# Optimization experiments

Measured on AMD Instinct MI355X. Metric: run time of the kernel, lower is better.

The kernel has to match this reference:

```python
import jax, jax.numpy as jnp
import numpy as np
from jax import lax

B = 32  # CS block size


def _conv(x, w, stride=1, pad=0):
    return lax.conv_general_dilated(
        x, w, window_strides=(stride, stride),
        padding=[(pad, pad), (pad, pad)],
        dimension_numbers=("NCHW", "OIHW", "NCHW"))


def _prelu(x, a):
    return jnp.where(x >= 0, x, a * x)


def _reshape_concat(x):
    # x: [N, B*B, h, w]; channel c = j*B + i maps to block pixel (i, j)
    # (tmp.view(B,B).permute(1,0) in the torch code). Blocks tile rows by
    # dim2 (h) and cols by dim3 (w). Vectorized depth-to-space + transpose.
    N, C, h, w = x.shape
    x5 = x.reshape(N, B, B, h, w)            # dims: (N, j, i, h, w)
    x5 = jnp.transpose(x5, (0, 3, 2, 4, 1))  # (N, h, i, w, j)
    return x5.reshape(N, 1, h * B, w * B)


def setup_inputs() -> dict:
    key = jax.random.key(0)
    ks = jax.random.split(key, 6)
    N, H, W = 16, 256, 256
    csnb = int(0.25 * B * B)  # 256
    inp = {
        "x": jax.random.normal(ks[0], (N, 1, H, W), jnp.float32),
        "W_cs": jax.random.normal(ks[1], (csnb, 1, B, B), jnp.float32) * 0.03,
        "W_init": jax.random.normal(ks[2], (B * B, csnb, 1, 1), jnp.float32) * 0.06,
        "W_first": jax.random.normal(ks[3], (64, 1, 3, 3), jnp.float32) * 0.3,
        "W_blk": jax.random.normal(ks[4], (64, 64, 3, 3), jnp.float32) * 0.04,
        "W_last": jax.random.normal(ks[5], (1, 64, 3, 3), jnp.float32) * 0.04,
        "a_main": jnp.full((1,), 0.1, jnp.float32),
        "a_blk": jnp.full((1,), 0.1, jnp.float32),
    }
    return inp


def reference(x, W_cs, W_init, W_first, W_blk, W_last, a_main, a_blk):
    # CS sampling: [N,1,H,W] -> [N,csnb,H/B,W/B]
    outcsy = _conv(x, W_cs, stride=B, pad=0)
    # initial reconstruction: 1x1 conv to B*B channels
    out = _conv(outcsy, W_init, stride=1, pad=0)
    out_initrec = _reshape_concat(out)          # [N,1,H,W]
    out = _prelu(_conv(out_initrec, W_first, pad=1), a_main)
    # same SORTRes_block (shared weights) applied 4 times
    for _ in range(4):
        o1 = _conv(out, W_blk, pad=1)
        o2 = _prelu(o1, a_blk)
        o3 = _conv(o2, W_blk, pad=1)
        out = _prelu(out + o3, a_blk)
    out = _conv(out + out_initrec, W_last, pad=1)
    return (out, outcsy, out_initrec)
```

## Files before the change

### kernel.cpp

```cpp
#include <hip/hip_runtime.h>
#include <hip/hip_bf16.h>
#include <initializer_list>


#define HW 65536
#define IMG 4194304

typedef __attribute__((ext_vector_type(8))) short short8;
typedef __attribute__((ext_vector_type(4))) float f32x4;

__device__ __forceinline__ float bf2f(unsigned short u) {
    union { unsigned u; float f; } v; v.u = ((unsigned)u) << 16; return v.f;
}
__device__ __forceinline__ unsigned short f2bf(float f) {
    union { float f; unsigned u; } v; v.f = f;
    unsigned r = v.u + 0x7FFF + ((v.u >> 16) & 1);
    return (unsigned short)(r >> 16);
}

__global__ void k_wcsT(const float* __restrict__ Wcs, float* __restrict__ WT)
{
    int e = blockIdx.x * 256 + threadIdx.x;
    int k = e >> 8, c = e & 255;
    WT[(long)k * 256 + c] = Wcs[(long)c * 1024 + k];
}

__global__ void k_winitT(const float* __restrict__ Wi, float* __restrict__ WT)
{
    int e = blockIdx.x * 256 + threadIdx.x;
    int ci = e >> 10, cc = e & 1023;
    WT[e] = Wi[(long)cc * 256 + ci];
}

__global__ __launch_bounds__(256) void k_cs2(const float* __restrict__ x,
        const float* __restrict__ WT, float* __restrict__ outcsy)
{
    __shared__ float xs[2][1024];
    const int b = blockIdx.x;
    const int tid = threadIdx.x;
#pragma unroll
    for (int t = 0; t < 2; ++t) {
        int p = b * 2 + t;
        int wb = p & 7, hb = (p >> 3) & 7, n = p >> 6;
#pragma unroll
        for (int i = 0; i < 4; ++i) {
            int k = tid + 256 * i;
            int ii = k >> 5, jj = k & 31;
            xs[t][k] = x[(long)n * HW + (hb * 32 + ii) * 256 + wb * 32 + jj];
        }
    }
    __syncthreads();
    float a0 = 0.f, a1 = 0.f;
    for (int k = 0; k < 1024; k += 8) {
#pragma unroll
        for (int u = 0; u < 8; ++u) {
            float wv = WT[(long)(k + u) * 256 + tid];
            a0 += wv * xs[0][k + u];
            a1 += wv * xs[1][k + u];
        }
    }
#pragma unroll
    for (int t = 0; t < 2; ++t) {
        int p = b * 2 + t;
        int wb = p & 7, hb = (p >> 3) & 7, n = p >> 6;
        float a = t ? a1 : a0;
        outcsy[(long)n * 16384 + tid * 64 + hb * 8 + wb] = a;
    }
}

__global__ __launch_bounds__(256) void k_init2(const float* __restrict__ outcsy,
        const float* __restrict__ WT, float* __restrict__ initrec)
{
    __shared__ float ys[2][256];
    __shared__ float ov[2][1024];
    const int b = blockIdx.x;
    const int np = b & 7, s = b >> 3;
    const int wb = s & 7, hb = s >> 3;
    const int tid = threadIdx.x;
#pragma unroll
    for (int i = 0; i < 2; ++i) {
        int idx = tid + 256 * i;
        int t = idx >> 8, c = idx & 255;
        ys[t][c] = outcsy[(long)(np * 2 + t) * 16384 + c * 64 + s];
    }
    __syncthreads();
#pragma unroll
    for (int q4 = 0; q4 < 4; ++q4) {
        int cc = q4 * 256 + tid;
        float a0 = 0.f, a1 = 0.f;
        for (int ci = 0; ci < 256; ci += 8) {
#pragma unroll
            for (int u = 0; u < 8; ++u) {
                float wv = WT[(long)(ci + u) * 1024 + cc];
                a0 += wv * ys[0][ci + u];
                a1 += wv * ys[1][ci + u];
            }
        }
        int i = cc & 31, j = cc >> 5;
        ov[0][i * 32 + j] = a0;
        ov[1][i * 32 + j] = a1;
    }
    __syncthreads();
#pragma unroll
    for (int t = 0; t < 2; ++t) {
        int n = np * 2 + t;
#pragma unroll
        for (int i2 = 0; i2 < 4; ++i2) {
            int p = i2 * 256 + tid;
            int i = p >> 5, j = p & 31;
            initrec[(long)n * HW + (hb * 32 + i) * 256 + wb * 32 + j] = ov[t][p];
        }
    }
}

__global__ __launch_bounds__(256) void k_first(const float* __restrict__ initrec,
        const float* __restrict__ Wf, unsigned short* __restrict__ A,
        const float* __restrict__ alpha_p)
{
    const int tid = threadIdx.x;
    const int w = tid >> 6, lane = tid & 63;
    const long p0 = (long)blockIdx.x * 64 + w * 16;
    const int n = (int)(p0 >> 16);
    const int y = (int)((p0 >> 8) & 255);
    const int xb = (int)(p0 & 255);
    float wf[9];
#pragma unroll
    for (int k = 0; k < 9; ++k) wf[k] = Wf[lane * 9 + k];
    const float alpha = alpha_p[0];
    const float* ip = initrec + (long)n * HW;
    for (int i = 0; i < 16; ++i) {
        int x = xb + i;
        float acc = 0.f;
#pragma unroll
        for (int ky = 0; ky < 3; ++ky) {
            int yy = y + ky - 1;
            if ((unsigned)yy >= 256u) continue;
#pragma unroll
            for (int kx = 0; kx < 3; ++kx) {
                int xx = x + kx - 1;
                if ((unsigned)xx >= 256u) continue;
                acc += wf[ky * 3 + kx] * ip[yy * 256 + xx];
            }
        }
        acc = acc >= 0.f ? acc : alpha * acc;
        A[(p0 + i) * 64 + lane] = f2bf(acc);
    }
}

__global__ void k_wprep(const float* __restrict__ Wb, unsigned short* __restrict__ Wp)
{
    int e = blockIdx.x * 256 + threadIdx.x;
    int cc = e / 18432, r = e % 18432;
    int tap = r / 2048, r2 = r % 2048;
    int nt = (r2 >> 9) & 3, l = (r2 >> 3) & 63, j = r2 & 7;
    int co = nt * 16 + (l & 15);
    int ci = cc * 32 + (l >> 4) * 8 + j;
    Wp[e] = f2bf(Wb[co * 576 + ci * 9 + tap]);
}

template <int MODE>
__global__ __launch_bounds__(256, 3) void k_conv(const unsigned short* __restrict__ src,
        const unsigned short* __restrict__ res, unsigned short* __restrict__ dst,
        const unsigned short* __restrict__ Wp, const float* __restrict__ alpha_p)
{
    __shared__ short halo[23328];

    const int tid = threadIdx.x;
    const int bid = blockIdx.x;
    const int tx = bid & 15, ty = (bid >> 4) & 15, n = bid >> 8;
    const int x0 = tx * 16, y0 = ty * 16;
    const int w = tid >> 6, lane = tid & 63;
    const int q = lane >> 4, mm = lane & 15;

    const unsigned short* sb = src + (long)n * IMG;
#pragma unroll
    for (int i = 0; i < 11; ++i) {
        int idx = tid + 256 * i;
        if (idx < 2592) {
            int pix = idx >> 3, part = idx & 7;
            int row = pix / 18, col = pix - row * 18;
            int gy = y0 + row - 1, gx = x0 + col - 1;
            short8 v = {0, 0, 0, 0, 0, 0, 0, 0};
            if ((unsigned)gy < 256u && (unsigned)gx < 256u)
                v = *(const short8*)&sb[((long)gy * 256 + gx) * 64 + part * 8];
            *(short8*)&halo[pix * 72 + part * 8] = v;
        }
    }

    short8 bcur[4], bnxt[4];
#pragma unroll
    for (int nt = 0; nt < 4; ++nt)
        bcur[nt] = *(const short8*)&Wp[(size_t)(nt * 512 + lane * 8)];

    const f32x4 zz = {0.f, 0.f, 0.f, 0.f};
    f32x4 acc[4][4];
#pragma unroll
    for (int mt = 0; mt < 4; ++mt)
#pragma unroll
        for (int nt = 0; nt < 4; ++nt) acc[mt][nt] = zz;

    __syncthreads();

    const int mmt = mm * 72 + q * 8;
#pragma unroll
    for (int s = 0; s < 18; ++s) {
        const int cc = s / 9, tap = s % 9;
        const int ky = tap / 3, kx = tap % 3;
        const int sn = (s + 1 < 18) ? s + 1 : s;
        const int ccn = sn / 9, tapn = sn % 9;
#pragma unroll
        for (int nt = 0; nt < 4; ++nt)
            bnxt[nt] = *(const short8*)&Wp[(size_t)ccn * 18432 +
                                           (size_t)((tapn * 4 + nt) * 512 + lane * 8)];
        const int soff = ky * 1296 + kx * 72 + cc * 32 + mmt;
#pragma unroll
        for (int mt = 0; mt < 4; ++mt) {
            short8 af = *(const short8*)&halo[(4 * w + mt) * 1296 + soff];
#pragma unroll
            for (int nt = 0; nt < 4; ++nt)
                acc[mt][nt] = __builtin_amdgcn_mfma_f32_16x16x32_bf16(
                    af, bcur[nt], acc[mt][nt], 0, 0, 0);
        }
#pragma unroll
        for (int nt = 0; nt < 4; ++nt) bcur[nt] = bnxt[nt];
    }
    __syncthreads();

    unsigned short* ob = (unsigned short*)halo;
    const float alpha = alpha_p[0];
#pragma unroll
    for (int h = 0; h < 2; ++h) {
        if ((w >> 1) == h) {
#pragma unroll
            for (int mt = 0; mt < 4; ++mt) {
                int row = 4 * w + mt - 8 * h;
#pragma unroll
                for (int nt = 0; nt < 4; ++nt)
#pragma unroll
                    for (int r = 0; r < 4; ++r) {
                        int xx = q * 4 + r;
                        ob[(row * 16 + xx) * 64 + nt * 16 + mm] = f2bf(acc[mt][nt][r]);
                    }
            }
        }
        __syncthreads();
#pragma unroll
        for (int i = 0; i < 4; ++i) {
            int e = (tid + 256 * i) * 8;
            int co = e & 63, xx = (e >> 6) & 15, row = 8 * h + (e >> 10);
            long g = (((long)n * 256 + y0 + row) * 256 + (x0 + xx)) * 64 + co;
            short8 cv = *(short8*)&ob[e];
            short8 rv = {0, 0, 0, 0, 0, 0, 0, 0};
            if (MODE == 1) rv = *(const short8*)&res[g];
            short8 ov;
#pragma unroll
            for (int j = 0; j < 8; ++j) {
                float v = bf2f((unsigned short)cv[j]);
                if (MODE == 1) v += bf2f((unsigned short)rv[j]);
                v = (v >= 0.f) ? v : alpha * v;
                ov[j] = (short)f2bf(v);
            }
            *(short8*)&dst[g] = ov;
        }
        __syncthreads();
    }
}

__global__ __launch_bounds__(256) void k_last(const unsigned short* __restrict__ A,
        const float* __restrict__ initrec, const float* __restrict__ Wl,
        float* __restrict__ out0)
{
    __shared__ short ibuf[23328];
    const int bid = blockIdx.x;
    const int tx = bid & 15, ty = (bid >> 4) & 15, n = bid >> 8;
    const int x0 = tx * 16, y0 = ty * 16;
    const int tid = threadIdx.x;
    const unsigned short* Ab = A + (long)n * IMG;

#pragma unroll
    for (int i = 0; i < 11; ++i) {
        int idx = tid + 256 * i;
        if (idx < 2592) {
            int pix = idx >> 3, part = idx & 7;
            int row = pix / 18, col = pix - row * 18;
            int gy = y0 + row - 1, gx = x0 + col - 1;
            short8 v = {0, 0, 0, 0, 0, 0, 0, 0};
            if ((unsigned)gy < 256u && (unsigned)gx < 256u)
                v = *(const short8*)&Ab[((long)gy * 256 + gx) * 64 + part * 8];
            *(short8*)&ibuf[pix * 72 + part * 8] = v;
        }
    }
    __syncthreads();

    float wsum[9];
#pragma unroll
    for (int k = 0; k < 9; ++k) wsum[k] = 0.f;
    for (int ci = 0; ci < 64; ++ci)
#pragma unroll
        for (int k = 0; k < 9; ++k) wsum[k] += Wl[ci * 9 + k];

    const int x = tid & 15, y = tid >> 4;
    const float* ip = initrec + (long)n * HW;
    float acc = 0.f;
#pragma unroll
    for (int ky = 0; ky < 3; ++ky) {
#pragma unroll
        for (int kx = 0; kx < 3; ++kx) {
            const int tap = ky * 3 + kx;
            const short* p = &ibuf[((y + ky) * 18 + (x + kx)) * 72];
#pragma unroll
            for (int c8 = 0; c8 < 8; ++c8) {
                short8 av = *(const short8*)&p[c8 * 8];
#pragma unroll
                for (int j = 0; j < 8; ++j)
                    acc += Wl[(c8 * 8 + j) * 9 + tap] * bf2f((unsigned short)av[j]);
            }
            int gy = y0 + y + ky - 1, gx = x0 + x + kx - 1;
            if ((unsigned)gy < 256u && (unsigned)gx < 256u)
                acc += wsum[tap] * ip[gy * 256 + gx];
        }
    }
    out0[((long)n * 256 + y0 + y) * 256 + (x0 + x)] = acc;
}

extern "C" void kernel_launch(void* const* d_in, const int* in_sizes, int n_in,
                              void* d_out, int out_size, void* d_ws, size_t ws_size,
                              hipStream_t stream)
{
    const float* x     = (const float*)d_in[0];
    const float* Wcs   = (const float*)d_in[1];
    const float* Winit = (const float*)d_in[2];
    const float* Wf    = (const float*)d_in[3];
    const float* Wb    = (const float*)d_in[4];
    const float* Wl    = (const float*)d_in[5];
    const float* amain = (const float*)d_in[6];
    const float* ablk  = (const float*)d_in[7];

    float* out0    = (float*)d_out;
    float* outcsy  = out0 + 1048576;
    float* initrec = outcsy + 262144;

    const size_t EXTRA = 73728 + 2 * 1048576;
    unsigned short* A = (unsigned short*)d_ws;
    int nc = 1;
    for (int c : {16, 8, 4, 2, 1})
        if ((size_t)(16 + c) * IMG * 2 + EXTRA <= ws_size) { nc = c; break; }
    unsigned short* Bt   = A + (size_t)16 * IMG;
    unsigned short* Wp   = Bt + (size_t)nc * IMG;
    float*          WcsT = (float*)(Wp + 36864);
    float*          WinT = WcsT + 262144;

    k_wcsT<<<1024, 256, 0, stream>>>(Wcs, WcsT);
    k_winitT<<<1024, 256, 0, stream>>>(Winit, WinT);
    k_wprep<<<144, 256, 0, stream>>>(Wb, Wp);

    k_cs2<<<512, 256, 0, stream>>>(x, WcsT, outcsy);
    k_init2<<<512, 256, 0, stream>>>(outcsy, WinT, initrec);
    k_first<<<16384, 256, 0, stream>>>(initrec, Wf, A, amain);

    for (int i = 0; i < 4; ++i) {
        for (int n0 = 0; n0 < 16; n0 += nc) {
            unsigned short* Ac = A + (size_t)n0 * IMG;
            k_conv<0><<<nc * 256, 256, 0, stream>>>(Ac, (const unsigned short*)nullptr,
                                                    Bt, Wp, ablk);
            k_conv<1><<<nc * 256, 256, 0, stream>>>(Bt, Ac, Ac, Wp, ablk);
        }
    }
    k_last<<<4096, 256, 0, stream>>>(A, initrec, Wl, out0);
}
```

Before: 1.235 ms.

## Fuse both convolutions of each residual block into one kernel with recomputed halo

Replaces the two per-block conv launches with a single kernel that loads a 20x20 halo tile in two 32-channel halves. It computes the first conv plus PReLU over an 18x18 region into shared memory, then runs the second conv from that buffer and applies the residual add and PReLU. This drops the global write and reread of the intermediate activation, and the blocks now ping-pong between two buffers. The cost is recomputing the halo ring (about 27% extra MFMA work on the first conv), more shared memory and lower occupancy. k_first is also rewritten so each thread handles one pixel and all 64 channels, writing them with vectorized 16-byte stores.

Result: faster. 1.125 ms (-9.0%).

```diff
diff --git a/kernel.cpp b/kernel.cpp
--- a/kernel.cpp
+++ b/kernel.cpp
@@ -117,33 +117,37 @@
         const float* __restrict__ Wf, unsigned short* __restrict__ A,
         const float* __restrict__ alpha_p)
 {
+    const int bid = blockIdx.x;
+    const int tx = bid & 15, ty = (bid >> 4) & 15, n = bid >> 8;
     const int tid = threadIdx.x;
-    const int w = tid >> 6, lane = tid & 63;
-    const long p0 = (long)blockIdx.x * 64 + w * 16;
-    const int n = (int)(p0 >> 16);
-    const int y = (int)((p0 >> 8) & 255);
-    const int xb = (int)(p0 & 255);
-    float wf[9];
-#pragma unroll
-    for (int k = 0; k < 9; ++k) wf[k] = Wf[lane * 9 + k];
+    const int x = (tx << 4) + (tid & 15), y = (ty << 4) + (tid >> 4);
+    const float* ip = initrec + (long)n * HW;
+
+    float in[9];
+#pragma unroll
+    for (int ky = 0; ky < 3; ++ky)
+#pragma unroll
+        for (int kx = 0; kx < 3; ++kx) {
+            int iy = y + ky - 1, ix = x + kx - 1;
+            in[ky * 3 + kx] = ((unsigned)iy < 256u && (unsigned)ix < 256u)
+                                  ? ip[iy * 256 + ix] : 0.f;
+        }
+
     const float alpha = alpha_p[0];
-    const float* ip = initrec + (long)n * HW;
-    for (int i = 0; i < 16; ++i) {
-        int x = xb + i;
-        float acc = 0.f;
-#pragma unroll
-        for (int ky = 0; ky < 3; ++ky) {
-            int yy = y + ky - 1;
-            if ((unsigned)yy >= 256u) continue;
-#pragma unroll
-            for (int kx = 0; kx < 3; ++kx) {
-                int xx = x + kx - 1;
-                if ((unsigned)xx >= 256u) continue;
-                acc += wf[ky * 3 + kx] * ip[yy * 256 + xx];
-            }
-        }
-        acc = acc >= 0.f ? acc : alpha * acc;
-        A[(p0 + i) * 64 + lane] = f2bf(acc);
+    unsigned short* op = &A[(((long)n * 256 + y) * 256 + x) * 64];
+#pragma unroll
+    for (int c8 = 0; c8 < 8; ++c8) {
+        short8 ov;
+#pragma unroll
+        for (int j = 0; j < 8; ++j) {
+            const float* wp = &Wf[(c8 * 8 + j) * 9];
+            float a = 0.f;
+#pragma unroll
+            for (int t = 0; t < 9; ++t) a += wp[t] * in[t];
+            a = a >= 0.f ? a : alpha * a;
+            ov[j] = (short)f2bf(a);
+        }
+        *(short8*)&op[c8 * 8] = ov;
     }
 }
 
@@ -158,12 +162,12 @@
     Wp[e] = f2bf(Wb[co * 576 + ci * 9 + tap]);
 }
 
-template <int MODE>
-__global__ __launch_bounds__(256, 3) void k_conv(const unsigned short* __restrict__ src,
-        const unsigned short* __restrict__ res, unsigned short* __restrict__ dst,
-        const unsigned short* __restrict__ Wp, const float* __restrict__ alpha_p)
-{
-    __shared__ short halo[23328];
+__global__ __launch_bounds__(256, 2) void k_res(const unsigned short* __restrict__ src,
+        unsigned short* __restrict__ dst, const unsigned short* __restrict__ Wp,
+        const float* __restrict__ alpha_p)
+{
+    __shared__ short halo[16000];
+    __shared__ short o2b[23328];
 
     const int tid = threadIdx.x;
     const int bid = blockIdx.x;
@@ -171,20 +175,15 @@
     const int x0 = tx * 16, y0 = ty * 16;
     const int w = tid >> 6, lane = tid & 63;
     const int q = lane >> 4, mm = lane & 15;
-
+    const float alpha = alpha_p[0];
     const unsigned short* sb = src + (long)n * IMG;
-#pragma unroll
-    for (int i = 0; i < 11; ++i) {
-        int idx = tid + 256 * i;
-        if (idx < 2592) {
-            int pix = idx >> 3, part = idx & 7;
-            int row = pix / 18, col = pix - row * 18;
-            int gy = y0 + row - 1, gx = x0 + col - 1;
-            short8 v = {0, 0, 0, 0, 0, 0, 0, 0};
-            if ((unsigned)gy < 256u && (unsigned)gx < 256u)
-                v = *(const short8*)&sb[((long)gy * 256 + gx) * 64 + part * 8];
-            *(short8*)&halo[pix * 72 + part * 8] = v;
-        }
+
+    int pb1[6];
+#pragma unroll
+    for (int i = 0; i < 6; ++i) {
+        int p = (w + 4 * i) * 16 + mm;
+        p = p < 323 ? p : 323;
+        pb1[i] = p + 2 * (p / 18);
     }
 
     short8 bcur[4], bnxt[4];
@@ -193,41 +192,107 @@
         bcur[nt] = *(const short8*)&Wp[(size_t)(nt * 512 + lane * 8)];
 
     const f32x4 zz = {0.f, 0.f, 0.f, 0.f};
-    f32x4 acc[4][4];
+    f32x4 acc1[6][4];
+#pragma unroll
+    for (int i = 0; i < 6; ++i)
+#pragma unroll
+        for (int nt = 0; nt < 4; ++nt) acc1[i][nt] = zz;
+
+    for (int cc = 0; cc < 2; ++cc) {
+        if (cc) __syncthreads();
+#pragma unroll
+        for (int i = 0; i < 7; ++i) {
+            int idx = tid + 256 * i;
+            if (idx < 1600) {
+                int pix = idx >> 2, part = idx & 3;
+                int row = pix / 20, col = pix - row * 20;
+                int gy = y0 + row - 2, gx = x0 + col - 2;
+                short8 v = {0, 0, 0, 0, 0, 0, 0, 0};
+                if ((unsigned)gy < 256u && (unsigned)gx < 256u)
+                    v = *(const short8*)&sb[((long)gy * 256 + gx) * 64 + cc * 32 + part * 8];
+                *(short8*)&halo[pix * 40 + part * 8] = v;
+            }
+        }
+        __syncthreads();
+
+#pragma unroll
+        for (int tap = 0; tap < 9; ++tap) {
+            const int s = cc * 9 + tap;
+            const int sn = (s + 1) % 18;
+            const int ccn = sn / 9, tapn = sn % 9;
+#pragma unroll
+            for (int nt = 0; nt < 4; ++nt)
+                bnxt[nt] = *(const short8*)&Wp[(size_t)ccn * 18432 +
+                                               (size_t)((tapn * 4 + nt) * 512 + lane * 8)];
+            const int ky = tap / 3, kx = tap % 3;
+            const int toff = (ky * 20 + kx) * 40 + q * 8;
+#pragma unroll
+            for (int i = 0; i < 6; ++i) {
+                short8 af = *(const short8*)&halo[pb1[i] * 40 + toff];
+#pragma unroll
+                for (int nt = 0; nt < 4; ++nt)
+                    acc1[i][nt] = __builtin_amdgcn_mfma_f32_16x16x32_bf16(
+                        af, bcur[nt], acc1[i][nt], 0, 0, 0);
+            }
+#pragma unroll
+            for (int nt = 0; nt < 4; ++nt) bcur[nt] = bnxt[nt];
+        }
+    }
+
+#pragma unroll
+    for (int i = 0; i < 6; ++i) {
+        int t = w + 4 * i;
+        if (t < 21) {
+#pragma unroll
+            for (int r = 0; r < 4; ++r) {
+                int p = t * 16 + q * 4 + r;
+                p = p < 323 ? p : 323;
+                int rho = p / 18, gam = p - 18 * rho;
+                bool valid = (unsigned)(y0 - 1 + rho) < 256u &&
+                             (unsigned)(x0 - 1 + gam) < 256u;
+#pragma unroll
+                for (int nt = 0; nt < 4; ++nt) {
+                    float v = acc1[i][nt][r];
+                    v = v >= 0.f ? v : alpha * v;
+                    o2b[p * 72 + nt * 16 + mm] = valid ? (short)f2bf(v) : (short)0;
+                }
+            }
+        }
+    }
+    __syncthreads();
+
+    f32x4 acc2[4][4];
 #pragma unroll
     for (int mt = 0; mt < 4; ++mt)
 #pragma unroll
-        for (int nt = 0; nt < 4; ++nt) acc[mt][nt] = zz;
-
-    __syncthreads();
-
-    const int mmt = mm * 72 + q * 8;
-#pragma unroll
-    for (int s = 0; s < 18; ++s) {
-        const int cc = s / 9, tap = s % 9;
-        const int ky = tap / 3, kx = tap % 3;
-        const int sn = (s + 1 < 18) ? s + 1 : s;
-        const int ccn = sn / 9, tapn = sn % 9;
-#pragma unroll
-        for (int nt = 0; nt < 4; ++nt)
-            bnxt[nt] = *(const short8*)&Wp[(size_t)ccn * 18432 +
-                                           (size_t)((tapn * 4 + nt) * 512 + lane * 8)];
-        const int soff = ky * 1296 + kx * 72 + cc * 32 + mmt;
-#pragma unroll
-        for (int mt = 0; mt < 4; ++mt) {
-            short8 af = *(const short8*)&halo[(4 * w + mt) * 1296 + soff];
+        for (int nt = 0; nt < 4; ++nt) acc2[mt][nt] = zz;
+
+    for (int cc = 0; cc < 2; ++cc) {
+#pragma unroll
+        for (int tap = 0; tap < 9; ++tap) {
+            const int s = cc * 9 + tap;
+            const int sn = (s + 1) % 18;
 #pragma unroll
             for (int nt = 0; nt < 4; ++nt)
-                acc[mt][nt] = __builtin_amdgcn_mfma_f32_16x16x32_bf16(
-                    af, bcur[nt], acc[mt][nt], 0, 0, 0);
-        }
-#pragma unroll
-        for (int nt = 0; nt < 4; ++nt) bcur[nt] = bnxt[nt];
-    }
-    __syncthreads();
-
-    unsigned short* ob = (unsigned short*)halo;
-    const float alpha = alpha_p[0];
+                bnxt[nt] = *(const short8*)&Wp[(size_t)(sn / 9) * 18432 +
+                                               (size_t)(((sn % 9) * 4 + nt) * 512 + lane * 8)];
+            const int ky = tap / 3, kx = tap % 3;
+#pragma unroll
+            for (int mt = 0; mt < 4; ++mt) {
+                short8 af = *(const short8*)&o2b[((4 * w + mt + ky) * 18 + mm + kx) * 72 +
+                                                 cc * 32 + q * 8];
+#pragma unroll
+                for (int nt = 0; nt < 4; ++nt)
+                    acc2[mt][nt] = __builtin_amdgcn_mfma_f32_16x16x32_bf16(
+                        af, bcur[nt], acc2[mt][nt], 0, 0, 0);
+            }
+#pragma unroll
+            for (int nt = 0; nt < 4; ++nt) bcur[nt] = bnxt[nt];
+        }
+    }
+    __syncthreads();
+
+    unsigned short* ob = (unsigned short*)o2b;
 #pragma unroll
     for (int h = 0; h < 2; ++h) {
         if ((w >> 1) == h) {
@@ -239,7 +304,7 @@
 #pragma unroll
                     for (int r = 0; r < 4; ++r) {
                         int xx = q * 4 + r;
-                        ob[(row * 16 + xx) * 64 + nt * 16 + mm] = f2bf(acc[mt][nt][r]);
+                        ob[(row * 16 + xx) * 64 + nt * 16 + mm] = f2bf(acc2[mt][nt][r]);
                     }
             }
         }
@@ -250,17 +315,16 @@
             int co = e & 63, xx = (e >> 6) & 15, row = 8 * h + (e >> 10);
             long g = (((long)n * 256 + y0 + row) * 256 + (x0 + xx)) * 64 + co;
             short8 cv = *(short8*)&ob[e];
-            short8 rv = {0, 0, 0, 0, 0, 0, 0, 0};
-            if (MODE == 1) rv = *(const short8*)&res[g];
+            short8 rv = *(const short8*)&src[(long)n * IMG +
+                                             ((long)(y0 + row) * 256 + x0 + xx) * 64 + co];
             short8 ov;
 #pragma unroll
             for (int j = 0; j < 8; ++j) {
-                float v = bf2f((unsigned short)cv[j]);
-                if (MODE == 1) v += bf2f((unsigned short)rv[j]);
+                float v = bf2f((unsigned short)cv[j]) + bf2f((unsigned short)rv[j]);
                 v = (v >= 0.f) ? v : alpha * v;
                 ov[j] = (short)f2bf(v);
             }
-            *(short8*)&dst[g] = ov;
+            *(short8*)&dst[(long)n * IMG + ((long)(y0 + row) * 256 + x0 + xx) * 64 + co] = ov;
         }
         __syncthreads();
     }
@@ -356,14 +420,14 @@
 
     k_cs2<<<512, 256, 0, stream>>>(x, WcsT, outcsy);
     k_init2<<<512, 256, 0, stream>>>(outcsy, WinT, initrec);
-    k_first<<<16384, 256, 0, stream>>>(initrec, Wf, A, amain);
-
-    for (int i = 0; i < 4; ++i) {
-        for (int n0 = 0; n0 < 16; n0 += nc) {
-            unsigned short* Ac = A + (size_t)n0 * IMG;
-            k_conv<0><<<nc * 256, 256, 0, stream>>>(Ac, (const unsigned short*)nullptr,
-                                                    Bt, Wp, ablk);
-            k_conv<1><<<nc * 256, 256, 0, stream>>>(Bt, Ac, Ac, Wp, ablk);
+    k_first<<<4096, 256, 0, stream>>>(initrec, Wf, A, amain);
+
+    for (int n0 = 0; n0 < 16; n0 += nc) {
+        unsigned short* Ac = A + (size_t)n0 * IMG;
+        for (int i = 0; i < 4; ++i) {
+            const unsigned short* s = (i & 1) ? Bt : Ac;
+            unsigned short*       d = (i & 1) ? Ac : Bt;
+            k_res<<<nc * 256, 256, 0, stream>>>(s, d, Wp, ablk);
         }
     }
     k_last<<<4096, 256, 0, stream>>>(A, initrec, Wl, out0);
```
